# Performance work log

Hardware: AMD Instinct MI355X
Metric: run time of the kernel (lower is better)

## Reference

```python
import jax, jax.numpy as jnp
import numpy as np


def setup_inputs() -> dict:
    key = jax.random.key(0)
    k0, k1, k2, k3, k4, k5 = jax.random.split(key, 6)
    T, B, V, L, H = 128, 128, 128000, 2, 1024  # seq_length, beam_size, vocab, layers, hidden
    return {
        "logprobsf": jax.random.normal(k0, (B, V), dtype=jnp.float32),
        "beam_seq": jax.random.randint(k1, (T, B), 0, V, dtype=jnp.int32),
        "beam_seq_logprobs": jax.random.normal(k2, (T, B), dtype=jnp.float32),
        "beam_logprob_sum": jax.random.normal(k3, (B,), dtype=jnp.float32),
        "state_h": jax.random.normal(k4, (L, B, H), dtype=jnp.float32),
        "state_c": jax.random.normal(k5, (L, B, H), dtype=jnp.float32),
        "t": 64,
        "beam_size": 128,
    }


def reference(logprobsf, beam_seq, beam_seq_logprobs, beam_logprob_sum, state_h, state_c, t, beam_size):
    """Vectorized, faithful beam_step (incl. the -1000 EOS penalty applied each
    timestep in beam_search before the step). t and beam_size are static ints."""
    V = logprobsf.shape[1]
    lp = logprobsf.at[:, V - 1].add(-1000.0)  # suppress EOS column

    cols = min(beam_size, V)
    rows = beam_size if t >= 1 else 1  # at t==0 all beams are identical

    # torch.sort descending + take first `cols` columns == top_k per row
    ys, ix = jax.lax.top_k(lp[:rows], cols)  # [rows, cols]

    # candidate total logprob for every (q, c) pair; pick global top beam_size
    cand_p = beam_logprob_sum[:rows, None] + ys  # [rows, cols]
    top_p, flat = jax.lax.top_k(cand_p.reshape(-1), beam_size)
    q_sel = flat // cols  # source beam per new beam
    c_sel = flat % cols   # rank within source beam's top-k

    tok = ix[q_sel, c_sel]  # chosen token ids, [beam_size]
    loc = ys[q_sel, c_sel]  # chosen local logprobs, [beam_size]

    # reorder beam history by source beam, then append step t
    new_seq = beam_seq.at[:t].set(beam_seq[:t, q_sel]).at[t].set(tok)
    new_logps = beam_seq_logprobs.at[:t].set(beam_seq_logprobs[:t, q_sel]).at[t].set(loc)
    new_sum = top_p

    # gather recurrent state along the beam dimension
    new_h = state_h[:, q_sel]
    new_c = state_c[:, q_sel]
    return new_seq, new_logps, new_sum, new_h, new_c
```

## Files before the change

kernel.cpp:

```cpp
#include <hip/hip_runtime.h>
#include <stdint.h>


#define SHIST 4096
#define CAP 32768
#define LCAP 256
#define FINCAP 512

typedef unsigned long long u64;

__device__ __forceinline__ unsigned f2key(float f) {
  unsigned u = __float_as_uint(f);
  return (u & 0x80000000u) ? ~u : (u | 0x80000000u);
}
__device__ __forceinline__ float key2f(unsigned k) {
  unsigned u = (k & 0x80000000u) ? (k & 0x7fffffffu) : ~k;
  return __uint_as_float(u);
}

__device__ __forceinline__ void suffix_thresh(unsigned* h , unsigned* seg ,
                                              unsigned target, int* sh_bin,
                                              unsigned* sh_above, int tid) {
  unsigned s = 0;
#pragma unroll
  for (int j = 0; j < SHIST / 256; ++j) s += h[tid * (SHIST / 256) + j];
  seg[tid] = s;
  __syncthreads();
  for (int off = 1; off < 256; off <<= 1) {
    unsigned add = (tid + off < 256) ? seg[tid + off] : 0;
    __syncthreads();
    seg[tid] += add;
    __syncthreads();
  }
  unsigned excl = (tid + 1 < 256) ? seg[tid + 1] : 0;
  unsigned incl = seg[tid];
  if (tid == 0) { *sh_bin = 0; *sh_above = 0; }
  __syncthreads();
  if (excl < target && incl >= target) {
    unsigned acc = excl;
    int lo = tid * (SHIST / 256);
    for (int bn = lo + SHIST / 256 - 1; bn >= lo; --bn) {
      unsigned hb = h[bn];
      if (acc + hb >= target) { *sh_bin = bn; *sh_above = acc; break; }
      acc += hb;
    }
  }
  __syncthreads();
}

extern "C" __global__ void __launch_bounds__(256)
k_sample(const float* __restrict__ logp, const float* __restrict__ bsum,
         const int* __restrict__ tptr, int V, int bs,
         unsigned* __restrict__ shist) {
  __shared__ unsigned hist[SHIST];
  for (int i = threadIdx.x; i < SHIST; i += 256) hist[i] = 0;
  __syncthreads();
  int t = *tptr;
  int rows = (t >= 1) ? bs : 1;
  long long total = (long long)rows * V;
  long long step = total / gridDim.x;
  long long start = (long long)blockIdx.x * step;
  int tid = threadIdx.x;
#pragma unroll 4
  for (int j = 0; j < 16; ++j) {
    long long idx = start + (long long)j * 256 + tid;
    if (idx < total) {
      int b = (int)(idx / V);
      int v = (int)(idx - (long long)b * V);
      float x = logp[idx];
      if (v == V - 1) x -= 1000.0f;
      atomicAdd(&hist[f2key(bsum[b] + x) >> 20], 1u);
    }
  }
  __syncthreads();
  for (int i = tid; i < SHIST; i += 256) {
    unsigned c = hist[i];
    if (c) atomicAdd(&shist[i], c);
  }
}

extern "C" __global__ void __launch_bounds__(256)
k_pick(const unsigned* __restrict__ shist, int K, unsigned* __restrict__ tlo_key) {
  __shared__ unsigned h[SHIST];
  __shared__ unsigned seg[256];
  __shared__ int sh_bin;
  __shared__ unsigned sh_above;
  int tid = threadIdx.x;
  for (int i = tid; i < SHIST; i += 256) h[i] = shist[i];
  __syncthreads();
  suffix_thresh(h, seg, (unsigned)K, &sh_bin, &sh_above, tid);
  if (tid == 0) *tlo_key = (unsigned)sh_bin << 20;
}

extern "C" __global__ void __launch_bounds__(256)
k_main(const float* __restrict__ logp, const float* __restrict__ bsum,
       const int* __restrict__ tptr, int V, int bs,
       const unsigned* __restrict__ tlo_p,
       u64* __restrict__ cand, int* __restrict__ cnt) {
  __shared__ u64 lbuf[LCAP];
  __shared__ int lcnt, lbase;
  int tid = threadIdx.x;
  if (tid == 0) lcnt = 0;
  __syncthreads();
  int t = *tptr;
  int rows = (t >= 1) ? bs : 1;
  unsigned tlo = *tlo_p;
  if ((V & 3) == 0) {
    unsigned V4 = (unsigned)V >> 2;
    unsigned total4 = (unsigned)rows * V4;
    unsigned stride = gridDim.x * 256;
    const float4* lp4 = (const float4*)logp;
    for (unsigned i = blockIdx.x * 256 + tid; i < total4; i += stride) {
      unsigned b = i / V4;
      unsigned v0 = (i - b * V4) << 2;
      float4 f = lp4[i];
      float s = bsum[b];
      float xs[4] = {f.x, f.y, f.z, f.w};
      if (v0 + 3 == (unsigned)V - 1) xs[3] -= 1000.0f;
#pragma unroll
      for (int j = 0; j < 4; ++j) {
        unsigned key = f2key(s + xs[j]);
        if (key >= tlo) {
          int p = atomicAdd(&lcnt, 1);
          if (p < LCAP) {
            unsigned flat = b * (unsigned)V + v0 + j;
            lbuf[p] = ((u64)key << 32) | (0xFFFFFFFFu - flat);
          }
        }
      }
    }
  } else {
    long long total = (long long)rows * V;
    long long stride = (long long)gridDim.x * 256;
    for (long long i = (long long)blockIdx.x * 256 + tid; i < total; i += stride) {
      int b = (int)(i / V);
      int v = (int)(i - (long long)b * V);
      float x = logp[i];
      if (v == V - 1) x -= 1000.0f;
      unsigned key = f2key(bsum[b] + x);
      if (key >= tlo) {
        int p = atomicAdd(&lcnt, 1);
        if (p < LCAP) {
          unsigned flat = (unsigned)b * (unsigned)V + (unsigned)v;
          lbuf[p] = ((u64)key << 32) | (0xFFFFFFFFu - flat);
        }
      }
    }
  }
  __syncthreads();
  int n = lcnt < LCAP ? lcnt : LCAP;
  if (tid == 0) lbase = atomicAdd(cnt, n);
  __syncthreads();
  int base = lbase;
  for (int i = tid; i < n; i += 256) {
    int g = base + i;
    if (g < CAP) cand[g] = lbuf[i];
  }
}

extern "C" __global__ void __launch_bounds__(256)
k_select(const float* __restrict__ logp, const int* __restrict__ cntp,
         const u64* __restrict__ cand_g, int V, int K,
         float* __restrict__ out_sum, int* __restrict__ qsel,
         int* __restrict__ tok, float* __restrict__ loc) {
  __shared__ unsigned hist[SHIST];
  __shared__ unsigned seg[256];
  __shared__ u64 fin[FINCAP];
  __shared__ int sh_bin, sh_nfin;
  __shared__ unsigned sh_above;
  int tid = threadIdx.x;
  int n = *cntp;
  if (n > CAP) n = CAP;
  for (int i = tid; i < SHIST; i += 256) hist[i] = 0;
  if (tid == 0) sh_nfin = 0;
  __syncthreads();
  for (int i = tid; i < n; i += 256)
    atomicAdd(&hist[(unsigned)(cand_g[i] >> 52)], 1u);
  __syncthreads();
  suffix_thresh(hist, seg, (unsigned)K, &sh_bin, &sh_above, tid);
  int tbin = sh_bin;
  unsigned cnt_hi = sh_above;
  __syncthreads();
  for (int i = tid; i < SHIST; i += 256) hist[i] = 0;
  __syncthreads();
  for (int i = tid; i < n; i += 256) {
    unsigned key = (unsigned)(cand_g[i] >> 32);
    if ((int)(key >> 20) == tbin) atomicAdd(&hist[(key >> 8) & 0xFFFu], 1u);
  }
  __syncthreads();
  unsigned need = (unsigned)K - cnt_hi;
  suffix_thresh(hist, seg, need, &sh_bin, &sh_above, tid);
  int tbin2 = sh_bin;
  __syncthreads();
  for (int i = tid; i < n; i += 256) {
    u64 c = cand_g[i];
    unsigned key = (unsigned)(c >> 32);
    int bin = (int)(key >> 20);
    bool keep = (bin > tbin) || (bin == tbin && (int)((key >> 8) & 0xFFFu) >= tbin2);
    if (keep) {
      int p = atomicAdd(&sh_nfin, 1);
      if (p < FINCAP) fin[p] = c;
    }
  }
  __syncthreads();
  int nf = sh_nfin < FINCAP ? sh_nfin : FINCAP;
  int m = 2;
  while (m < nf) m <<= 1;
  for (int i = nf + tid; i < m; i += 256) fin[i] = 0ull;
  __syncthreads();
  for (int k2 = 2; k2 <= m; k2 <<= 1) {
    for (int j = k2 >> 1; j > 0; j >>= 1) {
      for (int i = tid; i < m; i += 256) {
        int l = i ^ j;
        if (l > i) {
          u64 ai = fin[i], al = fin[l];
          bool desc = ((i & k2) == 0);
          if (desc ? (ai < al) : (ai > al)) { fin[i] = al; fin[l] = ai; }
        }
      }
      __syncthreads();
    }
  }
  if (tid < K) {
    u64 c = fin[tid];
    unsigned key = (unsigned)(c >> 32);
    unsigned flat = 0xFFFFFFFFu - (unsigned)(c & 0xFFFFFFFFull);
    int b = (int)(flat / (unsigned)V);
    int v = (int)(flat - (unsigned)b * (unsigned)V);
    out_sum[tid] = key2f(key);
    qsel[tid] = b;
    tok[tid] = v;
    float x = logp[(size_t)b * V + v];
    if (v == V - 1) x -= 1000.0f;
    loc[tid] = x;
  }
}

extern "C" __global__ void __launch_bounds__(256)
k_scatter(const int* __restrict__ beam_seq, const float* __restrict__ beam_lp,
          const float4* __restrict__ h4, const float4* __restrict__ c4,
          const int* __restrict__ tptr, const int* __restrict__ qsel,
          const int* __restrict__ tok, const float* __restrict__ loc,
          int T, int B, int LBH4, int H4,
          float* __restrict__ out, float4* __restrict__ outh4,
          float4* __restrict__ outc4) {
  int t = *tptr;
  size_t n_seq = (size_t)T * B;
  size_t scalar_items = 2 * n_seq;
  size_t total = scalar_items + 2 * (size_t)LBH4;
  size_t stride = (size_t)gridDim.x * 256;
  for (size_t j = (size_t)blockIdx.x * 256 + threadIdx.x; j < total; j += stride) {
    if (j < n_seq) {
      int ss = (int)(j / B), b = (int)(j % B);
      int val;
      if (ss < t)       val = beam_seq[(size_t)ss * B + qsel[b]];
      else if (ss == t) val = tok[b];
      else              val = beam_seq[j];
      out[j] = (float)val;
    } else if (j < scalar_items) {
      size_t jj = j - n_seq;
      int ss = (int)(jj / B), b = (int)(jj % B);
      float v;
      if (ss < t)       v = beam_lp[(size_t)ss * B + qsel[b]];
      else if (ss == t) v = loc[b];
      else              v = beam_lp[jj];
      out[j] = v;
    } else {
      size_t jj = j - scalar_items;
      bool is_c = jj >= (size_t)LBH4;
      size_t k = is_c ? jj - (size_t)LBH4 : jj;
      int row = (int)(k / H4);
      int h = (int)(k - (size_t)row * H4);
      int b = row % B;
      size_t src = (size_t)(row - b + qsel[b]) * H4 + h;
      if (is_c) outc4[k] = c4[src];
      else      outh4[k] = h4[src];
    }
  }
}

extern "C" void kernel_launch(void* const* d_in, const int* in_sizes, int n_in,
                              void* d_out, int out_size, void* d_ws, size_t ws_size,
                              hipStream_t stream) {
  const float* logp = (const float*)d_in[0];
  const int* beam_seq = (const int*)d_in[1];
  const float* beam_lp = (const float*)d_in[2];
  const float* bsum = (const float*)d_in[3];
  const float* st_h = (const float*)d_in[4];
  const float* st_c = (const float*)d_in[5];
  const int* tptr = (const int*)d_in[6];

  int B = in_sizes[3];
  int V = in_sizes[0] / B;
  int T = in_sizes[1] / B;
  int LBH = in_sizes[4];
  int LH = LBH / B;
  int bs = (out_size - 2 * in_sizes[1]) / (1 + 2 * LH);
  int H = 1024;
  int H4 = H / 4, LBH4 = LBH / 4;

  char* ws = (char*)d_ws;
  unsigned* shist = (unsigned*)ws;
  int* cnt = (int*)(ws + 16384);
  unsigned* tlo_key = (unsigned*)(ws + 16388);
  u64* cand = (u64*)(ws + 16392);
  int* qsel = (int*)(ws + 16392 + CAP * 8);
  int* tok = qsel + bs;
  float* loc = (float*)(tok + bs);

  float* out = (float*)d_out;
  size_t n_seq = (size_t)T * B;
  float* out_sum = out + 2 * n_seq;
  float4* outh4 = (float4*)(out + 2 * n_seq + bs);
  float4* outc4 = outh4 + LBH4;

  hipMemsetAsync(d_ws, 0, 16392, stream);
  k_sample<<<256, 256, 0, stream>>>(logp, bsum, tptr, V, bs, shist);
  k_pick<<<1, 256, 0, stream>>>(shist, bs, tlo_key);
  k_main<<<1024, 256, 0, stream>>>(logp, bsum, tptr, V, bs, tlo_key, cand, cnt);
  k_select<<<1, 256, 0, stream>>>(logp, cnt, cand, V, bs, out_sum, qsel, tok, loc);

  size_t total = 2 * n_seq + 2 * (size_t)LBH4;
  int blocks = (int)((total + 255) / 256);
  k_scatter<<<blocks, 256, 0, stream>>>(beam_seq, beam_lp,
                                        (const float4*)st_h, (const float4*)st_c,
                                        tptr, qsel, tok, loc,
                                        T, B, LBH4, H4, out, outh4, outc4);
}
```

Measured before the change: 157.7 us.

## Fold threshold pick into main filter kernel and use contiguous per-block chunks

Removes the single-block k_pick launch by having every k_main block load the sampled histogram and compute the threshold bin itself. The main scan switches from grid-stride to contiguous per-block chunks, uses nontemporal vector loads, and runs on 2048 blocks. The local candidate buffer grows to 1024 entries. In exchange each block redundantly does a 4096-entry histogram load and suffix scan, and uses more shared memory, which may lower occupancy.

```diff
diff --git a/kernel.cpp b/kernel.cpp
--- a/kernel.cpp
+++ b/kernel.cpp
@@ -4,10 +4,11 @@
 
 #define SHIST 4096
 #define CAP 32768
-#define LCAP 256
+#define LCAP 1024
 #define FINCAP 512
 
 typedef unsigned long long u64;
+typedef float f32x4 __attribute__((ext_vector_type(4)));
 
 __device__ __forceinline__ unsigned f2key(float f) {
   unsigned u = __float_as_uint(f);
@@ -80,40 +81,36 @@
 }
 
 extern "C" __global__ void __launch_bounds__(256)
-k_pick(const unsigned* __restrict__ shist, int K, unsigned* __restrict__ tlo_key) {
-  __shared__ unsigned h[SHIST];
+k_main(const float* __restrict__ logp, const float* __restrict__ bsum,
+       const int* __restrict__ tptr, int V, int bs,
+       const unsigned* __restrict__ shist,
+       u64* __restrict__ cand, int* __restrict__ cnt) {
+  __shared__ unsigned hist[SHIST];
   __shared__ unsigned seg[256];
-  __shared__ int sh_bin;
+  __shared__ u64 lbuf[LCAP];
+  __shared__ int lcnt, lbase, sh_bin;
   __shared__ unsigned sh_above;
   int tid = threadIdx.x;
-  for (int i = tid; i < SHIST; i += 256) h[i] = shist[i];
-  __syncthreads();
-  suffix_thresh(h, seg, (unsigned)K, &sh_bin, &sh_above, tid);
-  if (tid == 0) *tlo_key = (unsigned)sh_bin << 20;
-}
-
-extern "C" __global__ void __launch_bounds__(256)
-k_main(const float* __restrict__ logp, const float* __restrict__ bsum,
-       const int* __restrict__ tptr, int V, int bs,
-       const unsigned* __restrict__ tlo_p,
-       u64* __restrict__ cand, int* __restrict__ cnt) {
-  __shared__ u64 lbuf[LCAP];
-  __shared__ int lcnt, lbase;
-  int tid = threadIdx.x;
   if (tid == 0) lcnt = 0;
-  __syncthreads();
+  for (int i = tid; i < SHIST; i += 256) hist[i] = shist[i];
+  __syncthreads();
+  suffix_thresh(hist, seg, (unsigned)bs, &sh_bin, &sh_above, tid);
+  unsigned tlo = (unsigned)sh_bin << 20;
+
   int t = *tptr;
   int rows = (t >= 1) ? bs : 1;
-  unsigned tlo = *tlo_p;
   if ((V & 3) == 0) {
     unsigned V4 = (unsigned)V >> 2;
     unsigned total4 = (unsigned)rows * V4;
-    unsigned stride = gridDim.x * 256;
-    const float4* lp4 = (const float4*)logp;
-    for (unsigned i = blockIdx.x * 256 + tid; i < total4; i += stride) {
+    unsigned chunk = (total4 + gridDim.x - 1) / gridDim.x;
+    unsigned start = blockIdx.x * chunk;
+    unsigned end = start + chunk;
+    if (end > total4) end = total4;
+    const f32x4* lp4 = (const f32x4*)logp;
+    for (unsigned i = start + tid; i < end; i += 256) {
       unsigned b = i / V4;
       unsigned v0 = (i - b * V4) << 2;
-      float4 f = lp4[i];
+      f32x4 f = __builtin_nontemporal_load(&lp4[i]);
       float s = bsum[b];
       float xs[4] = {f.x, f.y, f.z, f.w};
       if (v0 + 3 == (unsigned)V - 1) xs[3] -= 1000.0f;
@@ -131,8 +128,11 @@
     }
   } else {
     long long total = (long long)rows * V;
-    long long stride = (long long)gridDim.x * 256;
-    for (long long i = (long long)blockIdx.x * 256 + tid; i < total; i += stride) {
+    long long chunk = (total + gridDim.x - 1) / gridDim.x;
+    long long start = (long long)blockIdx.x * chunk;
+    long long end = start + chunk;
+    if (end > total) end = total;
+    for (long long i = start + tid; i < end; i += 256) {
       int b = (int)(i / V);
       int v = (int)(i - (long long)b * V);
       float x = logp[i];
@@ -302,7 +302,6 @@
   char* ws = (char*)d_ws;
   unsigned* shist = (unsigned*)ws;
   int* cnt = (int*)(ws + 16384);
-  unsigned* tlo_key = (unsigned*)(ws + 16388);
   u64* cand = (u64*)(ws + 16392);
   int* qsel = (int*)(ws + 16392 + CAP * 8);
   int* tok = qsel + bs;
@@ -316,8 +315,7 @@
 
   hipMemsetAsync(d_ws, 0, 16392, stream);
   k_sample<<<256, 256, 0, stream>>>(logp, bsum, tptr, V, bs, shist);
-  k_pick<<<1, 256, 0, stream>>>(shist, bs, tlo_key);
-  k_main<<<1024, 256, 0, stream>>>(logp, bsum, tptr, V, bs, tlo_key, cand, cnt);
+  k_main<<<2048, 256, 0, stream>>>(logp, bsum, tptr, V, bs, shist, cand, cnt);
   k_select<<<1, 256, 0, stream>>>(logp, cnt, cand, V, bs, out_sum, qsel, tok, loc);
 
   size_t total = 2 * n_seq + 2 * (size_t)LBH4;
```

Result: slower. 177.7 us (+12.6%).
